# Kernel optimization log

Hardware: AMD Instinct MI355X
Metric: run time of the kernel (lower is better)

Reference implementation:

```python
import jax, jax.numpy as jnp
import numpy as np

CLAMP_MIN = 1e-6
CLAMP_MAX = 1e6


def setup_inputs() -> dict:
    key = jax.random.key(0)
    k1, k2, k3, k4, k5 = jax.random.split(key, 5)
    R, F, K = 4096, 256, 8
    return {
        "x1": jax.random.normal(k1, (R, F), dtype=jnp.float32),
        "x2": jax.random.normal(k2, (R, F), dtype=jnp.float32),
        "sigmas": jax.random.normal(k3, (K,), dtype=jnp.float32) * 100.0,
        "means": jax.random.normal(k4, (K,), dtype=jnp.float32),
        "sigma_parameters": jax.random.normal(k5, (K,), dtype=jnp.float32),
    }


def reference(x1, x2, sigmas, means, sigma_parameters):
    # dist_k[i,j] = sum_f (x1[i,f] - x2[j,f] - mean_k)^2
    #            = ||x1_i - x2_j||^2 - 2*mean_k*sum_f(x1_i - x2_j) + F*mean_k^2
    # Expansion avoids materializing the R x R x F broadcast tensor.
    R, F = x1.shape
    base = (
        jnp.sum(x1 * x1, axis=1)[:, None]
        + jnp.sum(x2 * x2, axis=1)[None, :]
        - 2.0 * (x1 @ x2.T)
    )  # [R, R]
    s = jnp.sum(x1, axis=1)[:, None] - jnp.sum(x2, axis=1)[None, :]  # [R, R]

    mean = means[:, None, None]  # [K,1,1]
    dist = base[None] - 2.0 * mean * s[None] + jnp.float32(F) * mean * mean  # [K,R,R]
    dist = jnp.clip(dist, CLAMP_MIN, CLAMP_MAX)

    kernel_value = jnp.exp(-dist / (2.0 * sigmas[:, None, None] ** 2))  # [K,R,R]
    softmaxed = jax.nn.softmax(kernel_value, axis=2)  # torch softmax(dim=1) per [R,R]

    weights = 1.0 / (sigma_parameters ** 2)
    normalized_weights = jax.nn.softmax(weights)  # softmax over K
    return jnp.sum(softmaxed * normalized_weights[:, None, None], axis=0)  # [R, R]
```

## Files before the change

kernel.cpp:

```cpp
#include <hip/hip_runtime.h>
#include <cmath>

#define R 4096
#define F 256
#define NK 8

typedef _Float16 half8 __attribute__((ext_vector_type(8)));
typedef _Float16 half4v __attribute__((ext_vector_type(4)));
typedef float f32x4 __attribute__((ext_vector_type(4)));

#define LOG2E      1.4426950408889634f
#define LOG2LOG2E  0.5287663729448977f


__global__ __launch_bounds__(256) void prep_kernel(
    const float* __restrict__ x1, const float* __restrict__ x2,
    const float* __restrict__ sigmas, const float* __restrict__ means,
    const float* __restrict__ sigp,
    _Float16* __restrict__ x1h, _Float16* __restrict__ x2h,
    float* __restrict__ rA, float* __restrict__ cB,
    float* __restrict__ S, float* __restrict__ prm)
{
    const int tid  = threadIdx.x;
    const int wid  = tid >> 6;
    const int lane = tid & 63;
    const int row  = blockIdx.x * 4 + wid;

    const float* src; _Float16* dsth; int r; bool isX1;
    if (row < R) { src = x1; dsth = x1h; r = row;     isX1 = true;  }
    else         { src = x2; dsth = x2h; r = row - R; isX1 = false; }

    float4 v = ((const float4*)(src + (size_t)r * F))[lane];
    half4v h = { (_Float16)v.x, (_Float16)v.y, (_Float16)v.z, (_Float16)v.w };
    *(half4v*)(dsth + (size_t)r * F + lane * 4) = h;

    float s = v.x + v.y + v.z + v.w;
    float q = v.x * v.x + v.y * v.y + v.z * v.z + v.w * v.w;
    for (int m = 1; m < 64; m <<= 1) {
        s += __shfl_xor(s, m);
        q += __shfl_xor(q, m);
    }
    if (lane < NK) {
        int k = lane;
        float sg = sigmas[k], m = means[k];
        float c  = -LOG2E / (2.f * sg * sg);
        if (isX1) rA[k * R + r] = c * (q - 2.f * m * s + (float)F * m * m) + LOG2LOG2E;
        else      cB[k * R + r] = c * (q + 2.f * m * s);
    }

    int g = blockIdx.x * 256 + tid;
    if (g < NK * R) S[g] = 0.f;

    if (blockIdx.x == 0 && tid == 0) {
        float w[NK], mx = -1e30f;
        for (int k = 0; k < NK; ++k) { float sp = sigp[k]; w[k] = 1.f / (sp * sp); mx = fmaxf(mx, w[k]); }
        float sum = 0.f;
        for (int k = 0; k < NK; ++k) { w[k] = expf(w[k] - mx); sum += w[k]; }
        for (int k = 0; k < NK; ++k) prm[k] = w[k] / sum;
        for (int k = 0; k < NK; ++k) {
            float sg = sigmas[k];
            prm[8 + k] = LOG2E / (sg * sg);
        }
    }
}

template <int PHASE>
__global__ __launch_bounds__(256, 2) void gemm_kernel(
    const _Float16* __restrict__ Ah, const _Float16* __restrict__ Bh,
    const float* __restrict__ rA, const float* __restrict__ cB,
    const float* __restrict__ prm, float* __restrict__ S, float* __restrict__ out)
{
    constexpr int SK = 72;
    __shared__ _Float16 As[128 * SK];
    __shared__ _Float16 Bs[128 * SK];

    const int tid  = threadIdx.x;
    const int lane = tid & 63;
    const int wid  = tid >> 6;
    const int wm   = wid >> 1, wn = wid & 1;
    const int q    = lane >> 4, m16 = lane & 15;
    const int tm   = blockIdx.y, tn = blockIdx.x;

    f32x4 acc[4][4];
#pragma unroll
    for (int a = 0; a < 4; ++a)
#pragma unroll
        for (int b = 0; b < 4; ++b)
            acc[a][b] = (f32x4){0.f, 0.f, 0.f, 0.f};

    for (int k0 = 0; k0 < F; k0 += 64) {
#pragma unroll
        for (int c = 0; c < 4; ++c) {
            int idx = c * 256 + tid;
            int row = idx >> 3, c8 = (idx & 7) * 8;
            *(uint4*)&As[row * SK + c8] =
                *(const uint4*)&Ah[(size_t)(tm * 128 + row) * F + k0 + c8];
            *(uint4*)&Bs[row * SK + c8] =
                *(const uint4*)&Bh[(size_t)(tn * 128 + row) * F + k0 + c8];
        }
        __syncthreads();
#pragma unroll
        for (int s = 0; s < 2; ++s) {
            half8 a[4], b[4];
#pragma unroll
            for (int mt = 0; mt < 4; ++mt)
                a[mt] = *(const half8*)&As[(wm * 64 + mt * 16 + m16) * SK + s * 32 + q * 8];
#pragma unroll
            for (int nt = 0; nt < 4; ++nt)
                b[nt] = *(const half8*)&Bs[(wn * 64 + nt * 16 + m16) * SK + s * 32 + q * 8];
#pragma unroll
            for (int mt = 0; mt < 4; ++mt)
#pragma unroll
                for (int nt = 0; nt < 4; ++nt)
                    acc[mt][nt] = __builtin_amdgcn_mfma_f32_16x16x32_f16(
                        a[mt], b[nt], acc[mt][nt], 0, 0, 0);
        }
        __syncthreads();
    }

    float g[8], wv[8];
#pragma unroll
    for (int k = 0; k < 8; ++k) g[k] = prm[8 + k];
    if (PHASE == 1) {
#pragma unroll
        for (int k = 0; k < 8; ++k) wv[k] = prm[k];
    }

    int colg[4];
    float colQ[8][4];
#pragma unroll
    for (int nt = 0; nt < 4; ++nt) {
        colg[nt] = tn * 128 + wn * 64 + nt * 16 + m16;
#pragma unroll
        for (int k = 0; k < 8; ++k) colQ[k][nt] = cB[k * R + colg[nt]];
    }

#pragma unroll
    for (int mt = 0; mt < 4; ++mt) {
#pragma unroll
        for (int r = 0; r < 4; ++r) {
            int rowg = tm * 128 + wm * 64 + mt * 16 + q * 4 + r;
            float rAv[8];
#pragma unroll
            for (int k = 0; k < 8; ++k) rAv[k] = rA[k * R + rowg];

            if (PHASE == 0) {
#pragma unroll
                for (int k = 0; k < 8; ++k) {
                    float t = 0.f;
#pragma unroll
                    for (int nt = 0; nt < 4; ++nt) {
                        float tt = fmaf(g[k], acc[mt][nt][r], rAv[k] + colQ[k][nt]);
                        t += __builtin_amdgcn_exp2f(__builtin_amdgcn_exp2f(tt));
                    }
                    t += __shfl_xor(t, 1); t += __shfl_xor(t, 2);
                    t += __shfl_xor(t, 4); t += __shfl_xor(t, 8);
                    if (m16 == 0) atomicAdd(&S[k * R + rowg], t);
                }
            } else {
                float sv[8];
#pragma unroll
                for (int k = 0; k < 8; ++k)
                    sv[k] = wv[k] * __builtin_amdgcn_rcpf(S[k * R + rowg]);
#pragma unroll
                for (int nt = 0; nt < 4; ++nt) {
                    float d = acc[mt][nt][r];
                    float o = 0.f;
#pragma unroll
                    for (int k = 0; k < 8; ++k) {
                        float tt = fmaf(g[k], d, rAv[k] + colQ[k][nt]);
                        o = fmaf(sv[k], __builtin_amdgcn_exp2f(__builtin_amdgcn_exp2f(tt)), o);
                    }
                    __builtin_nontemporal_store(o, &out[(size_t)rowg * R + colg[nt]]);
                }
            }
        }
    }
}

extern "C" void kernel_launch(void* const* d_in, const int* in_sizes, int n_in,
                              void* d_out, int out_size, void* d_ws, size_t ws_size,
                              hipStream_t stream) {
    (void)in_sizes; (void)n_in; (void)out_size; (void)ws_size;
    const float* x1     = (const float*)d_in[0];
    const float* x2     = (const float*)d_in[1];
    const float* sigmas = (const float*)d_in[2];
    const float* means  = (const float*)d_in[3];
    const float* sigp   = (const float*)d_in[4];
    float* out = (float*)d_out;

    char* ws = (char*)d_ws;
    _Float16* x1h = (_Float16*)ws;
    _Float16* x2h = (_Float16*)(ws + 2097152);
    float* S   = (float*)(ws + 4194304);
    float* rA  = (float*)(ws + 4194304 + 131072);
    float* cB  = (float*)(ws + 4194304 + 262144);
    float* prm = (float*)(ws + 4194304 + 393216);

    prep_kernel<<<2048, 256, 0, stream>>>(x1, x2, sigmas, means, sigp,
                                          x1h, x2h, rA, cB, S, prm);
    gemm_kernel<0><<<dim3(32, 32), 256, 0, stream>>>(x1h, x2h, rA, cB, prm, S, out);
    gemm_kernel<1><<<dim3(32, 32), 256, 0, stream>>>(x1h, x2h, rA, cB, prm, S, out);
}
```

Before: 179.0 us.

## Use direct global-to-LDS loads with XOR swizzle, DPP reductions, plain stores

Tile staging now uses global_load_lds so data goes straight into shared memory, with an XOR-swizzled layout that replaces the padded layout to avoid bank conflicts. In phase 0 the shuffle-based row reduction becomes DPP adds and the rA loads are vectorized. Phase 1 now writes output with normal stores instead of nontemporal ones. The swizzle must stay consistent between the direct loads and the MFMA operand reads, and the DPP row_shr-style controls need to produce correct 16-lane sums.

```diff
diff --git a/kernel.cpp b/kernel.cpp
--- a/kernel.cpp
+++ b/kernel.cpp
@@ -64,67 +64,126 @@
     }
 }
 
-template <int PHASE>
-__global__ __launch_bounds__(256, 2) void gemm_kernel(
+template <int CTRL>
+__device__ __forceinline__ float dpp_radd(float x) {
+    int xi = __builtin_bit_cast(int, x);
+    int yi = __builtin_amdgcn_update_dpp(0, xi, CTRL, 0xF, 0xF, true);
+    return x + __builtin_bit_cast(float, yi);
+}
+
+__device__ __forceinline__ void gload_lds16(const void* g, void* l) {
+    __builtin_amdgcn_global_load_lds(
+        (const __attribute__((address_space(1))) void*)g,
+        (__attribute__((address_space(3))) void*)l, 16, 0, 0);
+}
+
+#define GEMM_BODY                                                             \
+    __shared__ _Float16 As[128 * 64];                                         \
+    __shared__ _Float16 Bs[128 * 64];                                         \
+    const int tid  = threadIdx.x;                                             \
+    const int lane = tid & 63;                                                \
+    const int wid  = tid >> 6;                                                \
+    const int wm   = wid >> 1, wn = wid & 1;          \
+    const int q    = lane >> 4, m16 = lane & 15;                              \
+    const int tm   = blockIdx.y, tn = blockIdx.x;                             \
+    const int srow  = tid >> 3;                        \
+    const int slot  = tid & 7;                       \
+    const int sslot = slot ^ (srow & 7);            \
+    f32x4 acc[4][4];                                                          \
+    _Pragma("unroll")                                                         \
+    for (int a = 0; a < 4; ++a)                                               \
+        _Pragma("unroll")                                                     \
+        for (int b = 0; b < 4; ++b)                                           \
+            acc[a][b] = (f32x4){0.f, 0.f, 0.f, 0.f};                          \
+    for (int k0 = 0; k0 < F; k0 += 64) {                                      \
+        _Pragma("unroll")                                                     \
+        for (int c = 0; c < 4; ++c) {                                         \
+            int row = c * 32 + srow;                                          \
+            gload_lds16(&Ah[(size_t)(tm * 128 + row) * F + k0 + sslot * 8],   \
+                        &As[row * 64 + slot * 8]);                            \
+            gload_lds16(&Bh[(size_t)(tn * 128 + row) * F + k0 + sslot * 8],   \
+                        &Bs[row * 64 + slot * 8]);                            \
+        }                                                                     \
+        __syncthreads();                                                      \
+        _Pragma("unroll")                                                     \
+        for (int s = 0; s < 2; ++s) {                                         \
+            half8 a[4], b[4];                                                 \
+            _Pragma("unroll")                                                 \
+            for (int mt = 0; mt < 4; ++mt) {                                  \
+                int ar = wm * 64 + mt * 16 + m16;                             \
+                a[mt] = *(const half8*)&As[ar * 64 +                          \
+                         (((s * 4 + q) ^ (ar & 7)) * 8)];                     \
+            }                                                                 \
+            _Pragma("unroll")                                                 \
+            for (int nt = 0; nt < 4; ++nt) {                                  \
+                int br = wn * 64 + nt * 16 + m16;                             \
+                b[nt] = *(const half8*)&Bs[br * 64 +                          \
+                         (((s * 4 + q) ^ (br & 7)) * 8)];                     \
+            }                                                                 \
+            _Pragma("unroll")                                                 \
+            for (int mt = 0; mt < 4; ++mt)                                    \
+                _Pragma("unroll")                                             \
+                for (int nt = 0; nt < 4; ++nt)                                \
+                    acc[mt][nt] = __builtin_amdgcn_mfma_f32_16x16x32_f16(     \
+                        a[mt], b[nt], acc[mt][nt], 0, 0, 0);                  \
+        }                                                                     \
+        __syncthreads();                                                      \
+    }
+
+__global__ __launch_bounds__(256, 2) void gemm_phase0(
     const _Float16* __restrict__ Ah, const _Float16* __restrict__ Bh,
     const float* __restrict__ rA, const float* __restrict__ cB,
-    const float* __restrict__ prm, float* __restrict__ S, float* __restrict__ out)
+    const float* __restrict__ prm, float* __restrict__ S)
 {
-    constexpr int SK = 72;
-    __shared__ _Float16 As[128 * SK];
-    __shared__ _Float16 Bs[128 * SK];
-
-    const int tid  = threadIdx.x;
-    const int lane = tid & 63;
-    const int wid  = tid >> 6;
-    const int wm   = wid >> 1, wn = wid & 1;
-    const int q    = lane >> 4, m16 = lane & 15;
-    const int tm   = blockIdx.y, tn = blockIdx.x;
-
-    f32x4 acc[4][4];
-#pragma unroll
-    for (int a = 0; a < 4; ++a)
-#pragma unroll
-        for (int b = 0; b < 4; ++b)
-            acc[a][b] = (f32x4){0.f, 0.f, 0.f, 0.f};
-
-    for (int k0 = 0; k0 < F; k0 += 64) {
-#pragma unroll
-        for (int c = 0; c < 4; ++c) {
-            int idx = c * 256 + tid;
-            int row = idx >> 3, c8 = (idx & 7) * 8;
-            *(uint4*)&As[row * SK + c8] =
-                *(const uint4*)&Ah[(size_t)(tm * 128 + row) * F + k0 + c8];
-            *(uint4*)&Bs[row * SK + c8] =
-                *(const uint4*)&Bh[(size_t)(tn * 128 + row) * F + k0 + c8];
+    GEMM_BODY
+
+    float g[8];
+#pragma unroll
+    for (int k = 0; k < 8; ++k) g[k] = prm[8 + k];
+
+    float colQ[8][4];
+#pragma unroll
+    for (int nt = 0; nt < 4; ++nt) {
+        int colg = tn * 128 + wn * 64 + nt * 16 + m16;
+#pragma unroll
+        for (int k = 0; k < 8; ++k) colQ[k][nt] = cB[k * R + colg];
+    }
+
+#pragma unroll
+    for (int mt = 0; mt < 4; ++mt) {
+        int rowb = tm * 128 + wm * 64 + mt * 16 + q * 4;
+#pragma unroll
+        for (int k = 0; k < 8; ++k) {
+            f32x4 ra4 = *(const f32x4*)&rA[k * R + rowb];
+#pragma unroll
+            for (int r = 0; r < 4; ++r) {
+                float t = 0.f;
+#pragma unroll
+                for (int nt = 0; nt < 4; ++nt) {
+                    float tt = fmaf(g[k], acc[mt][nt][r], ra4[r] + colQ[k][nt]);
+                    t += __builtin_amdgcn_exp2f(__builtin_amdgcn_exp2f(tt));
+                }
+                t = dpp_radd<0xB1>(t);
+                t = dpp_radd<0x4E>(t);
+                t = dpp_radd<0x124>(t);
+                t = dpp_radd<0x128>(t);
+                if (m16 == 0) atomicAdd(&S[k * R + rowb + r], t);
+            }
         }
-        __syncthreads();
-#pragma unroll
-        for (int s = 0; s < 2; ++s) {
-            half8 a[4], b[4];
-#pragma unroll
-            for (int mt = 0; mt < 4; ++mt)
-                a[mt] = *(const half8*)&As[(wm * 64 + mt * 16 + m16) * SK + s * 32 + q * 8];
-#pragma unroll
-            for (int nt = 0; nt < 4; ++nt)
-                b[nt] = *(const half8*)&Bs[(wn * 64 + nt * 16 + m16) * SK + s * 32 + q * 8];
-#pragma unroll
-            for (int mt = 0; mt < 4; ++mt)
-#pragma unroll
-                for (int nt = 0; nt < 4; ++nt)
-                    acc[mt][nt] = __builtin_amdgcn_mfma_f32_16x16x32_f16(
-                        a[mt], b[nt], acc[mt][nt], 0, 0, 0);
-        }
-        __syncthreads();
-    }
+    }
+}
+
+__global__ __launch_bounds__(256, 2) void gemm_phase1(
+    const _Float16* __restrict__ Ah, const _Float16* __restrict__ Bh,
+    const float* __restrict__ rA, const float* __restrict__ cB,
+    const float* __restrict__ prm, const float* __restrict__ S,
+    float* __restrict__ out)
+{
+    GEMM_BODY
 
     float g[8], wv[8];
 #pragma unroll
-    for (int k = 0; k < 8; ++k) g[k] = prm[8 + k];
-    if (PHASE == 1) {
-#pragma unroll
-        for (int k = 0; k < 8; ++k) wv[k] = prm[k];
-    }
+    for (int k = 0; k < 8; ++k) { g[k] = prm[8 + k]; wv[k] = prm[k]; }
 
     int colg[4];
     float colQ[8][4];
@@ -143,36 +202,20 @@
             float rAv[8];
 #pragma unroll
             for (int k = 0; k < 8; ++k) rAv[k] = rA[k * R + rowg];
-
-            if (PHASE == 0) {
+            float sv[8];
+#pragma unroll
+            for (int k = 0; k < 8; ++k)
+                sv[k] = wv[k] * __builtin_amdgcn_rcpf(S[k * R + rowg]);
+#pragma unroll
+            for (int nt = 0; nt < 4; ++nt) {
+                float d = acc[mt][nt][r];
+                float o = 0.f;
 #pragma unroll
                 for (int k = 0; k < 8; ++k) {
-                    float t = 0.f;
-#pragma unroll
-                    for (int nt = 0; nt < 4; ++nt) {
-                        float tt = fmaf(g[k], acc[mt][nt][r], rAv[k] + colQ[k][nt]);
-                        t += __builtin_amdgcn_exp2f(__builtin_amdgcn_exp2f(tt));
-                    }
-                    t += __shfl_xor(t, 1); t += __shfl_xor(t, 2);
-                    t += __shfl_xor(t, 4); t += __shfl_xor(t, 8);
-                    if (m16 == 0) atomicAdd(&S[k * R + rowg], t);
+                    float tt = fmaf(g[k], d, rAv[k] + colQ[k][nt]);
+                    o = fmaf(sv[k], __builtin_amdgcn_exp2f(__builtin_amdgcn_exp2f(tt)), o);
                 }
-            } else {
-                float sv[8];
-#pragma unroll
-                for (int k = 0; k < 8; ++k)
-                    sv[k] = wv[k] * __builtin_amdgcn_rcpf(S[k * R + rowg]);
-#pragma unroll
-                for (int nt = 0; nt < 4; ++nt) {
-                    float d = acc[mt][nt][r];
-                    float o = 0.f;
-#pragma unroll
-                    for (int k = 0; k < 8; ++k) {
-                        float tt = fmaf(g[k], d, rAv[k] + colQ[k][nt]);
-                        o = fmaf(sv[k], __builtin_amdgcn_exp2f(__builtin_amdgcn_exp2f(tt)), o);
-                    }
-                    __builtin_nontemporal_store(o, &out[(size_t)rowg * R + colg[nt]]);
-                }
+                out[(size_t)rowg * R + colg[nt]] = o;
             }
         }
     }
@@ -199,6 +242,6 @@
 
     prep_kernel<<<2048, 256, 0, stream>>>(x1, x2, sigmas, means, sigp,
                                           x1h, x2h, rA, cB, S, prm);
-    gemm_kernel<0><<<dim3(32, 32), 256, 0, stream>>>(x1h, x2h, rA, cB, prm, S, out);
-    gemm_kernel<1><<<dim3(32, 32), 256, 0, stream>>>(x1h, x2h, rA, cB, prm, S, out);
-}
+    gemm_phase0<<<dim3(32, 32), 256, 0, stream>>>(x1h, x2h, rA, cB, prm, S);
+    gemm_phase1<<<dim3(32, 32), 256, 0, stream>>>(x1h, x2h, rA, cB, prm, S, out);
+}
```

Result: slower. 186.0 us (+3.9%).
